# Performance work log

Hardware: AMD Instinct MI355X
Metric: run time of the kernel (lower is better)

Reference implementation:

```python
import jax, jax.numpy as jnp
import numpy as np

N = 524288
L = 16          # num_levels
F = 2           # per_level_dim
T = 1 << 19     # hashmap size per level
BASE, MAXR = 32, 2048
SCALE = np.exp(np.log(MAXR / BASE) / (L - 1))
RES = [int(np.floor(BASE * SCALE ** lv)) + 1 for lv in range(L)]
ACTIVE = 4 * F  # init_active_level * per_level_dim (progressive mask)
D_HID = 64
N_FREQS = 6

_P1 = jnp.uint32(2654435761)
_P2 = jnp.uint32(805459861)
_OFF = jnp.array([[(c >> d) & 1 for d in range(3)] for c in range(8)], dtype=jnp.uint32)  # [8,3]


def setup_inputs() -> dict:
    key = jax.random.key(0)
    ks = jax.random.split(key, 8)
    x = (jax.random.uniform(ks[0], (N, 3)) * 2.0 - 1.0) * 0.999  # inside [-bound, bound]
    v = jax.random.normal(ks[1], (N, 3))
    v = v / jnp.linalg.norm(v, axis=-1, keepdims=True)
    o = jax.random.normal(ks[2], (N, 3))  # unused by forward (kept for signature fidelity)
    table = jax.random.uniform(ks[3], (L, T, F), minval=-1e-4, maxval=1e-4)
    d_in = 3 + 3 * 2 * N_FREQS + L * F  # xyz + fourier + hashgrid = 71
    def lin(k, fi, fo):
        return jax.random.normal(k, (fi, fo)) * np.sqrt(2.0 / fi).astype(np.float32)
    dw1 = lin(ks[4], d_in, D_HID); db1 = jnp.zeros((D_HID,), jnp.float32)
    dw2 = lin(ks[5], D_HID, 1 + D_HID); db2 = jnp.zeros((1 + D_HID,), jnp.float32)
    rw1 = lin(ks[6], D_HID + 9, D_HID); rb1 = jnp.zeros((D_HID,), jnp.float32)
    rw2 = lin(ks[7], D_HID, 3); rb2 = jnp.zeros((3,), jnp.float32)
    return dict(x=x, v=v, o=o, table=table, dw1=dw1, db1=db1, dw2=dw2, db2=db2,
                rw1=rw1, rb1=rb1, rw2=rw2, rb2=rb2)


def hashgrid(x01, table):
    """Multi-res hash encoding with Smoothstep interpolation. x01 in [0,1]^3."""
    feats = []
    for lv in range(L):
        pos = x01 * RES[lv]
        p0 = jnp.floor(pos)
        t = pos - p0
        w = t * t * (3.0 - 2.0 * t)                       # smoothstep weights [N,3]
        corner = p0.astype(jnp.uint32)[:, None, :] + _OFF[None]  # [N,8,3]
        h = (corner[..., 0] ^ (corner[..., 1] * _P1) ^ (corner[..., 2] * _P2)) & jnp.uint32(T - 1)
        cw = jnp.prod(jnp.where(_OFF[None] == 1, w[:, None, :], 1.0 - w[:, None, :]), axis=-1)  # [N,8]
        feats.append(jnp.sum(table[lv][h.astype(jnp.int32)] * cw[..., None], axis=1))  # [N,F]
    return jnp.concatenate(feats, axis=-1)  # [N, L*F]


def fourier(x):
    freqs = 2.0 ** jnp.arange(N_FREQS, dtype=x.dtype)  # log-sampled 2^0..2^5
    ang = x[..., None] * freqs                         # [N,3,6]
    return jnp.concatenate([jnp.sin(ang), jnp.cos(ang)], axis=-1).reshape(x.shape[0], -1)


def sh3(d):
    """Spherical harmonics, degree 3 (levels=3) -> 9 features."""
    xx, yy, zz = d[..., 0], d[..., 1], d[..., 2]
    return jnp.stack([
        0.28209479177387814 * jnp.ones_like(xx),
        -0.4886025119029199 * yy, 0.4886025119029199 * zz, -0.4886025119029199 * xx,
        1.0925484305920792 * xx * yy, -1.0925484305920792 * yy * zz,
        0.9461746957575601 * zz * zz - 0.31539156525252005,
        -1.0925484305920792 * xx * zz,
        0.5462742152960396 * (xx * xx - yy * yy)], axis=-1)


def reference(x, v, o, table, dw1, db1, dw2, db2, rw1, rb1, rw2, rb2):
    x01 = (x + 1.0) * 0.5  # bound = 1.0
    grid = hashgrid(x01, table)
    mask = (jnp.arange(L * F) < ACTIVE).astype(grid.dtype)  # progressive level mask
    x_enc = jnp.concatenate([x, fourier(x), grid * mask], axis=-1)  # [N,71]
    h = jax.nn.relu(x_enc @ dw1 + db1)
    dout = h @ dw2 + db2                 # [N, 1 + d_hidden]
    sigma = jnp.exp(dout[..., :1])       # trunc_exp forward == exp
    feat = jax.nn.relu(dout[..., 1:])
    rgb_in = jnp.concatenate([feat, sh3(v)], axis=-1)  # [N, 73]
    hr = jax.nn.relu(rgb_in @ rw1 + rb1)
    rgb = jax.nn.sigmoid(hr @ rw2 + rb2)
    return sigma, rgb
```

## Files before the change

kernel.cpp:

```cpp
#include <hip/hip_runtime.h>

#define NPTS   524288
#define TBLM   ((1u << 19) - 1u)
#define THR    512
#define CHUNK  128
#define CHUNKS 4
#define GRID   (NPTS / (CHUNK * CHUNKS))

typedef _Float16 half8  __attribute__((ext_vector_type(8)));
typedef _Float16 half4v __attribute__((ext_vector_type(4)));
typedef _Float16 half2v __attribute__((ext_vector_type(2)));
typedef float    f32x4  __attribute__((ext_vector_type(4)));


__global__ __launch_bounds__(256)
void prep(const float* __restrict__ dw1, const float* __restrict__ db1,
          const float* __restrict__ dw2, const float* __restrict__ db2,
          const float* __restrict__ rw1, const float* __restrict__ rb1,
          const float* __restrict__ rw2, const float* __restrict__ rb2,
          void* __restrict__ ws)
{
    const int t = blockIdx.x * 256 + threadIdx.x;
    if (t < 16384) {
        float w = 0.0f;
        if (t < 4096) {
            const int u = t, mkc = u >> 9, m = mkc >> 1, kc = mkc & 1;
            const int lane = (u >> 3) & 63, j = u & 7;
            const int row = 16 * m + (lane & 15);
            const int kp  = kc * 32 + (lane >> 4) * 8 + j;
            if (kp < 39)      w = dw1[kp * 64 + row];
            else if (kp == 39) w = 0.0f;
            else if (kp < 48) w = dw1[(kp - 1) * 64 + row];
        } else if (t < 9216) {
            const int u = t - 4096, mkc = u >> 9, m = mkc >> 1, kc = mkc & 1;
            const int lane = (u >> 3) & 63, j = u & 7;
            const int row = 16 * m + (lane & 15);
            const int k   = kc * 32 + (lane >> 4) * 8 + j;
            if (row < 65) w = dw2[k * 65 + row];
        } else if (t < 15360) {
            const int u = t - 9216, mkc = u >> 9, m = mkc / 3, kc = mkc - 3 * m;
            const int lane = (u >> 3) & 63, j = u & 7;
            const int row = 16 * m + (lane & 15);
            const int kp  = kc * 32 + (lane >> 4) * 8 + j;
            if (kp >= 1 && kp <= 73) w = rw1[(kp - 1) * 64 + row];
        } else {
            const int u = t - 15360, kc = u >> 9;
            const int lane = (u >> 3) & 63, j = u & 7;
            const int row = lane & 15;
            const int k   = kc * 32 + (lane >> 4) * 8 + j;
            if (row < 3) w = rw2[k * 3 + row];
        }
        ((_Float16*)ws)[t] = (_Float16)w;
    } else if (t < 16384 + 224) {
        const int u = t - 16384;
        float b = 0.0f;
        if (u < 64)        b = db1[u];
        else if (u < 144)  { const int r = u - 64;  if (r < 65) b = db2[r]; }
        else if (u < 208)  b = rb1[u - 144];
        else               { const int r = u - 208; if (r < 3)  b = rb2[r]; }
        ((float*)((char*)ws + 32768))[u] = b;
    }
}

__device__ __forceinline__ float sstep(float t) { return t * t * (3.0f - 2.0f * t); }

struct GS {
    float  x0, x1, x2, v0, v1, v2;
    float  ax, ay, az;
    float2 t0, t1, t2, t3, t4, t5, t6, t7;
};

__device__ __forceinline__ void gather_issue(int gi, int role,
    const float* __restrict__ x, const float* __restrict__ v,
    const float* __restrict__ table, GS& s)
{
    s.x0 = x[3 * gi + 0]; s.x1 = x[3 * gi + 1]; s.x2 = x[3 * gi + 2];
    if (role == 1) { s.v0 = v[3 * gi + 0]; s.v1 = v[3 * gi + 1]; s.v2 = v[3 * gi + 2]; }
    const float rf = (role == 0) ? 33.f : (role == 1) ? 43.f : (role == 2) ? 56.f : 74.f;
    const float u0 = (s.x0 + 1.f) * 0.5f, u1 = (s.x1 + 1.f) * 0.5f, u2 = (s.x2 + 1.f) * 0.5f;
    const float px = u0 * rf, py = u1 * rf, pz = u2 * rf;
    const float fx = floorf(px), fy = floorf(py), fz = floorf(pz);
    s.ax = sstep(px - fx); s.ay = sstep(py - fy); s.az = sstep(pz - fz);
    const unsigned cx = (unsigned)fx, cy = (unsigned)fy, cz = (unsigned)fz;
    const float* tb = table + (unsigned)role * (TBLM + 1u) * 2u;
    const unsigned hy0 = cy * 2654435761u, hy1 = (cy + 1u) * 2654435761u;
    const unsigned hz0 = cz * 805459861u,  hz1 = (cz + 1u) * 805459861u;
#define LDC(dst, HX, HY, HZ) { const unsigned hh = ((HX) ^ (HY) ^ (HZ)) & TBLM; \
                               dst = *reinterpret_cast<const float2*>(tb + hh * 2u); }
    LDC(s.t0, cx,      hy0, hz0);
    LDC(s.t1, cx + 1u, hy0, hz0);
    LDC(s.t2, cx,      hy1, hz0);
    LDC(s.t3, cx + 1u, hy1, hz0);
    LDC(s.t4, cx,      hy0, hz1);
    LDC(s.t5, cx + 1u, hy0, hz1);
    LDC(s.t6, cx,      hy1, hz1);
    LDC(s.t7, cx + 1u, hy1, hz1);
#undef LDC
}

__device__ __forceinline__ void encode_finish(const GS& s, int role, _Float16* row)
{
    const float ax = s.ax, ay = s.ay, az = s.az;
    const float bx = 1.f - ax, by = 1.f - ay, bz = 1.f - az;
    const float p00 = bx * by, p10 = ax * by, p01 = bx * ay, p11 = ax * ay;
    const float w0 = p00 * bz, w1 = p10 * bz, w2 = p01 * bz, w3 = p11 * bz;
    const float w4 = p00 * az, w5 = p10 * az, w6 = p01 * az, w7 = p11 * az;
    float g0 = w0 * s.t0.x, g1 = w0 * s.t0.y;
    g0 = fmaf(w1, s.t1.x, g0); g1 = fmaf(w1, s.t1.y, g1);
    g0 = fmaf(w2, s.t2.x, g0); g1 = fmaf(w2, s.t2.y, g1);
    g0 = fmaf(w3, s.t3.x, g0); g1 = fmaf(w3, s.t3.y, g1);
    g0 = fmaf(w4, s.t4.x, g0); g1 = fmaf(w4, s.t4.y, g1);
    g0 = fmaf(w5, s.t5.x, g0); g1 = fmaf(w5, s.t5.y, g1);
    g0 = fmaf(w6, s.t6.x, g0); g1 = fmaf(w6, s.t6.y, g1);
    g0 = fmaf(w7, s.t7.x, g0); g1 = fmaf(w7, s.t7.y, g1);
    half2v gh; gh[0] = (_Float16)g0; gh[1] = (_Float16)g1;
    *(half2v*)(row + 40 + 2 * role) = gh;

    if (role == 0) {
        float e[40];
        e[0] = s.x0; e[1] = s.x1; e[2] = s.x2;
        const float a[3] = {s.x0, s.x1, s.x2};
        #pragma unroll
        for (int d = 0; d < 3; ++d)
            #pragma unroll
            for (int f = 0; f < 6; ++f) {
                const float ang = a[d] * (float)(1 << f);
                e[3 + d * 12 + f]     = __sinf(ang);
                e[3 + d * 12 + 6 + f] = __cosf(ang);
            }
        e[39] = 0.0f;
        #pragma unroll
        for (int chk = 0; chk < 5; ++chk) {
            half8 h;
            #pragma unroll
            for (int i = 0; i < 8; ++i) h[i] = (_Float16)e[chk * 8 + i];
            *(half8*)(row + chk * 8) = h;
        }
    } else if (role == 1) {
        const float v0 = s.v0, v1 = s.v1, v2 = s.v2;
        float sh[9];
        sh[0] = 0.28209479177387814f;
        sh[1] = -0.4886025119029199f * v1;
        sh[2] =  0.4886025119029199f * v2;
        sh[3] = -0.4886025119029199f * v0;
        sh[4] =  1.0925484305920792f * v0 * v1;
        sh[5] = -1.0925484305920792f * v1 * v2;
        sh[6] =  0.9461746957575601f * v2 * v2 - 0.31539156525252005f;
        sh[7] = -1.0925484305920792f * v0 * v2;
        sh[8] =  0.5462742152960396f * (v0 * v0 - v1 * v1);
        half8 s0, s1;
        s0[0] = (_Float16)0.f;
        #pragma unroll
        for (int i = 0; i < 7; ++i) s0[i + 1] = (_Float16)sh[i];
        s1[0] = (_Float16)sh[7]; s1[1] = (_Float16)sh[8];
        #pragma unroll
        for (int i = 2; i < 8; ++i) s1[i] = (_Float16)0.f;
        *(half8*)(row + 64) = s0;
        *(half8*)(row + 72) = s1;
    } else if (role == 2) {
        half8 z;
        #pragma unroll
        for (int i = 0; i < 8; ++i) z[i] = (_Float16)0.f;
        *(half8*)(row + 48) = z;
        *(half8*)(row + 56) = z;
    } else {
        half8 z;
        #pragma unroll
        for (int i = 0; i < 8; ++i) z[i] = (_Float16)0.f;
        *(half8*)(row + 80) = z;
        *(half8*)(row + 88) = z;
    }
}

__global__ __launch_bounds__(THR, 4)
void nerf_fwd(const float* __restrict__ x,
              const float* __restrict__ v,
              const float* __restrict__ table,
              const float* __restrict__ ws,
              float* __restrict__ out)
{
    __shared__ __align__(16) unsigned char smem[78720];
    _Float16* wt    = (_Float16*)smem;
    float*    sbias = (float*)(smem + 32768);
    _Float16* aB    = (_Float16*)(smem + 33664);
    _Float16* bB    = (_Float16*)(smem + 60288);

    const int tid  = threadIdx.x;
    const int lane = tid & 63;
    const int wv   = tid >> 6;
    const int lr   = lane & 15;
    const int lg   = lane >> 4;
    const int role = lane & 3;
    const int ep   = (wv << 4) + (lane >> 2);
    const int gi0  = blockIdx.x * (CHUNK * CHUNKS);

    GS cur, nxt;
    gather_issue(gi0 + ep, role, x, v, table, cur);

    {
        const uint4* src = (const uint4*)ws;
        uint4* dst = (uint4*)smem;
        #pragma unroll
        for (int i = 0; i < 5; ++i) {
            const int idx = tid + i * THR;
            if (idx < 2104) dst[idx] = src[idx];
        }
    }
    __syncthreads();

    const int pt = (wv << 4) + lr;

    #pragma unroll
    for (int c = 0; c < CHUNKS; ++c) {
        const int cbase = gi0 + c * CHUNK;

        encode_finish(cur, role, aB + ep * 104);

        if (c + 1 < CHUNKS)
            gather_issue(gi0 + (c + 1) * CHUNK + ep, role, x, v, table, nxt);

        {
            const half8 B0 = *(const half8*)(aB + pt * 104 + 0 * 32 + lg * 8);
            const half8 B1 = *(const half8*)(aB + pt * 104 + 1 * 32 + lg * 8);
            #pragma unroll
            for (int m = 0; m < 4; ++m) {
                const half8 A0 = *(const half8*)(wt + (m * 2 + 0) * 512 + lane * 8);
                const half8 A1 = *(const half8*)(wt + (m * 2 + 1) * 512 + lane * 8);
                f32x4 cr = *(const f32x4*)(sbias + 0 + m * 16 + 4 * lg);
                cr = __builtin_amdgcn_mfma_f32_16x16x32_f16(A0, B0, cr, 0, 0, 0);
                cr = __builtin_amdgcn_mfma_f32_16x16x32_f16(A1, B1, cr, 0, 0, 0);
                half4v o4;
                #pragma unroll
                for (int r = 0; r < 4; ++r) o4[r] = (_Float16)fmaxf(cr[r], 0.f);
                *(half4v*)(bB + pt * 72 + 16 * m + 4 * lg) = o4;
            }
        }

        {
            const half8 B0 = *(const half8*)(bB + pt * 72 + 0 * 32 + lg * 8);
            const half8 B1 = *(const half8*)(bB + pt * 72 + 1 * 32 + lg * 8);
            #pragma unroll
            for (int m = 0; m < 4; ++m) {
                const half8 A0 = *(const half8*)(wt + 4096 + (m * 2 + 0) * 512 + lane * 8);
                const half8 A1 = *(const half8*)(wt + 4096 + (m * 2 + 1) * 512 + lane * 8);
                f32x4 cr = *(const f32x4*)(sbias + 64 + m * 16 + 4 * lg);
                cr = __builtin_amdgcn_mfma_f32_16x16x32_f16(A0, B0, cr, 0, 0, 0);
                cr = __builtin_amdgcn_mfma_f32_16x16x32_f16(A1, B1, cr, 0, 0, 0);
                half4v o4;
                #pragma unroll
                for (int r = 0; r < 4; ++r) o4[r] = (_Float16)fmaxf(cr[r], 0.f);
                *(half4v*)(aB + pt * 104 + 16 * m + 4 * lg) = o4;
                if (m == 0 && lg == 0)
                    out[cbase + pt] = __expf(cr[0]);
            }
            {
                const half8 A0 = *(const half8*)(wt + 4096 + (4 * 2 + 0) * 512 + lane * 8);
                const half8 A1 = *(const half8*)(wt + 4096 + (4 * 2 + 1) * 512 + lane * 8);
                f32x4 cr = *(const f32x4*)(sbias + 64 + 4 * 16 + 4 * lg);
                cr = __builtin_amdgcn_mfma_f32_16x16x32_f16(A0, B0, cr, 0, 0, 0);
                cr = __builtin_amdgcn_mfma_f32_16x16x32_f16(A1, B1, cr, 0, 0, 0);
                if (lg == 0) aB[pt * 104 + 64] = (_Float16)fmaxf(cr[0], 0.f);
            }
        }

        {
            const half8 B0 = *(const half8*)(aB + pt * 104 + 0 * 32 + lg * 8);
            const half8 B1 = *(const half8*)(aB + pt * 104 + 1 * 32 + lg * 8);
            const half8 B2 = *(const half8*)(aB + pt * 104 + 2 * 32 + lg * 8);
            #pragma unroll
            for (int m = 0; m < 4; ++m) {
                const half8 A0 = *(const half8*)(wt + 9216 + (m * 3 + 0) * 512 + lane * 8);
                const half8 A1 = *(const half8*)(wt + 9216 + (m * 3 + 1) * 512 + lane * 8);
                const half8 A2 = *(const half8*)(wt + 9216 + (m * 3 + 2) * 512 + lane * 8);
                f32x4 cr = *(const f32x4*)(sbias + 144 + m * 16 + 4 * lg);
                cr = __builtin_amdgcn_mfma_f32_16x16x32_f16(A0, B0, cr, 0, 0, 0);
                cr = __builtin_amdgcn_mfma_f32_16x16x32_f16(A1, B1, cr, 0, 0, 0);
                cr = __builtin_amdgcn_mfma_f32_16x16x32_f16(A2, B2, cr, 0, 0, 0);
                half4v o4;
                #pragma unroll
                for (int r = 0; r < 4; ++r) o4[r] = (_Float16)fmaxf(cr[r], 0.f);
                *(half4v*)(bB + pt * 72 + 16 * m + 4 * lg) = o4;
            }
        }

        {
            const half8 A0 = *(const half8*)(wt + 15360 + 0 * 512 + lane * 8);
            const half8 A1 = *(const half8*)(wt + 15360 + 1 * 512 + lane * 8);
            const half8 B0 = *(const half8*)(bB + pt * 72 + 0 * 32 + lg * 8);
            const half8 B1 = *(const half8*)(bB + pt * 72 + 1 * 32 + lg * 8);
            f32x4 cr = *(const f32x4*)(sbias + 208 + 4 * lg);
            cr = __builtin_amdgcn_mfma_f32_16x16x32_f16(A0, B0, cr, 0, 0, 0);
            cr = __builtin_amdgcn_mfma_f32_16x16x32_f16(A1, B1, cr, 0, 0, 0);
            if (lg == 0) {
                const int gpt = cbase + pt;
                #pragma unroll
                for (int r = 0; r < 3; ++r)
                    out[NPTS + 3 * gpt + r] = 1.0f / (1.0f + __expf(-cr[r]));
            }
        }

        if (c + 1 < CHUNKS) cur = nxt;
    }
}

extern "C" void kernel_launch(void* const* d_in, const int* in_sizes, int n_in,
                              void* d_out, int out_size, void* d_ws, size_t ws_size,
                              hipStream_t stream) {
    const float* x     = (const float*)d_in[0];
    const float* v     = (const float*)d_in[1];
    const float* table = (const float*)d_in[3];
    const float* dw1   = (const float*)d_in[4];
    const float* db1   = (const float*)d_in[5];
    const float* dw2   = (const float*)d_in[6];
    const float* db2   = (const float*)d_in[7];
    const float* rw1   = (const float*)d_in[8];
    const float* rb1   = (const float*)d_in[9];
    const float* rw2   = (const float*)d_in[10];
    const float* rb2   = (const float*)d_in[11];
    float* out = (float*)d_out;

    hipLaunchKernelGGL(prep, dim3(65), dim3(256), 0, stream,
                       dw1, db1, dw2, db2, rw1, rb1, rw2, rb2, d_ws);
    hipLaunchKernelGGL(nerf_fwd, dim3(GRID), dim3(THR), 0, stream,
                       x, v, table, (const float*)d_ws, out);
}
```

Before: 187.8 us.

## Hold MLP weights in registers and shrink blocks to 256 threads

Loads all fp16 MLP weight fragments into per-lane registers once per block instead of reading them from LDS for every MFMA. LDS now holds only the biases and the activation buffers. Blocks shrink to 256 threads with 8 chunks of 64 points, and launch bounds drop to 2 blocks per CU. The zero-padding of activation rows is hoisted out of the per-chunk encode into a single pre-loop step. The aim is to cut LDS traffic and LDS footprint, at the cost of about 100 extra VGPRs per lane, which lowers occupancy and the latency hiding available for the hash-table gathers.

```diff
diff --git a/kernel.cpp b/kernel.cpp
--- a/kernel.cpp
+++ b/kernel.cpp
@@ -2,9 +2,9 @@
 
 #define NPTS   524288
 #define TBLM   ((1u << 19) - 1u)
-#define THR    512
-#define CHUNK  128
-#define CHUNKS 4
+#define THR    256
+#define CHUNK  64
+#define CHUNKS 8
 #define GRID   (NPTS / (CHUNK * CHUNKS))
 
 typedef _Float16 half8  __attribute__((ext_vector_type(8)));
@@ -157,33 +157,20 @@
         for (int i = 2; i < 8; ++i) s1[i] = (_Float16)0.f;
         *(half8*)(row + 64) = s0;
         *(half8*)(row + 72) = s1;
-    } else if (role == 2) {
-        half8 z;
-        #pragma unroll
-        for (int i = 0; i < 8; ++i) z[i] = (_Float16)0.f;
-        *(half8*)(row + 48) = z;
-        *(half8*)(row + 56) = z;
-    } else {
-        half8 z;
-        #pragma unroll
-        for (int i = 0; i < 8; ++i) z[i] = (_Float16)0.f;
-        *(half8*)(row + 80) = z;
-        *(half8*)(row + 88) = z;
     }
 }
 
-__global__ __launch_bounds__(THR, 4)
+__global__ __launch_bounds__(THR, 2)
 void nerf_fwd(const float* __restrict__ x,
               const float* __restrict__ v,
               const float* __restrict__ table,
               const float* __restrict__ ws,
               float* __restrict__ out)
 {
-    __shared__ __align__(16) unsigned char smem[78720];
-    _Float16* wt    = (_Float16*)smem;
-    float*    sbias = (float*)(smem + 32768);
-    _Float16* aB    = (_Float16*)(smem + 33664);
-    _Float16* bB    = (_Float16*)(smem + 60288);
+    __shared__ __align__(16) unsigned char smem[23424];
+    float*    sbias = (float*)smem;
+    _Float16* aB    = (_Float16*)(smem + 896);
+    _Float16* bB    = (_Float16*)(smem + 14208);
 
     const int tid  = threadIdx.x;
     const int lane = tid & 63;
@@ -197,20 +184,42 @@
     GS cur, nxt;
     gather_issue(gi0 + ep, role, x, v, table, cur);
 
+    const _Float16* wsH = (const _Float16*)ws;
+    half8 W1[4][2], W2[5][2], W3[4][3], W4[2];
+    #pragma unroll
+    for (int m = 0; m < 4; ++m)
+        #pragma unroll
+        for (int kc = 0; kc < 2; ++kc)
+            W1[m][kc] = *(const half8*)(wsH + (m * 2 + kc) * 512 + lane * 8);
+    #pragma unroll
+    for (int m = 0; m < 5; ++m)
+        #pragma unroll
+        for (int kc = 0; kc < 2; ++kc)
+            W2[m][kc] = *(const half8*)(wsH + 4096 + (m * 2 + kc) * 512 + lane * 8);
+    #pragma unroll
+    for (int m = 0; m < 4; ++m)
+        #pragma unroll
+        for (int kc = 0; kc < 3; ++kc)
+            W3[m][kc] = *(const half8*)(wsH + 9216 + (m * 3 + kc) * 512 + lane * 8);
+    #pragma unroll
+    for (int kc = 0; kc < 2; ++kc)
+        W4[kc] = *(const half8*)(wsH + 15360 + kc * 512 + lane * 8);
+
+    if (tid < 56) ((uint4*)sbias)[tid] = ((const uint4*)((const char*)ws + 32768))[tid];
+    __syncthreads();
+
     {
-        const uint4* src = (const uint4*)ws;
-        uint4* dst = (uint4*)smem;
-        #pragma unroll
-        for (int i = 0; i < 5; ++i) {
-            const int idx = tid + i * THR;
-            if (idx < 2104) dst[idx] = src[idx];
-        }
+        _Float16* rowp = aB + ep * 104;
+        half8 z;
+        #pragma unroll
+        for (int i = 0; i < 8; ++i) z[i] = (_Float16)0.f;
+        *(half8*)(rowp + 48 + 8 * role) = z;
+        if (role < 2) *(half8*)(rowp + 80 + 8 * role) = z;
     }
-    __syncthreads();
 
     const int pt = (wv << 4) + lr;
 
-    #pragma unroll
+    #pragma unroll 2
     for (int c = 0; c < CHUNKS; ++c) {
         const int cbase = gi0 + c * CHUNK;
 
@@ -224,11 +233,9 @@
             const half8 B1 = *(const half8*)(aB + pt * 104 + 1 * 32 + lg * 8);
             #pragma unroll
             for (int m = 0; m < 4; ++m) {
-                const half8 A0 = *(const half8*)(wt + (m * 2 + 0) * 512 + lane * 8);
-                const half8 A1 = *(const half8*)(wt + (m * 2 + 1) * 512 + lane * 8);
                 f32x4 cr = *(const f32x4*)(sbias + 0 + m * 16 + 4 * lg);
-                cr = __builtin_amdgcn_mfma_f32_16x16x32_f16(A0, B0, cr, 0, 0, 0);
-                cr = __builtin_amdgcn_mfma_f32_16x16x32_f16(A1, B1, cr, 0, 0, 0);
+                cr = __builtin_amdgcn_mfma_f32_16x16x32_f16(W1[m][0], B0, cr, 0, 0, 0);
+                cr = __builtin_amdgcn_mfma_f32_16x16x32_f16(W1[m][1], B1, cr, 0, 0, 0);
                 half4v o4;
                 #pragma unroll
                 for (int r = 0; r < 4; ++r) o4[r] = (_Float16)fmaxf(cr[r], 0.f);
@@ -241,11 +248,9 @@
             const half8 B1 = *(const half8*)(bB + pt * 72 + 1 * 32 + lg * 8);
             #pragma unroll
             for (int m = 0; m < 4; ++m) {
-                const half8 A0 = *(const half8*)(wt + 4096 + (m * 2 + 0) * 512 + lane * 8);
-                const half8 A1 = *(const half8*)(wt + 4096 + (m * 2 + 1) * 512 + lane * 8);
                 f32x4 cr = *(const f32x4*)(sbias + 64 + m * 16 + 4 * lg);
-                cr = __builtin_amdgcn_mfma_f32_16x16x32_f16(A0, B0, cr, 0, 0, 0);
-                cr = __builtin_amdgcn_mfma_f32_16x16x32_f16(A1, B1, cr, 0, 0, 0);
+                cr = __builtin_amdgcn_mfma_f32_16x16x32_f16(W2[m][0], B0, cr, 0, 0, 0);
+                cr = __builtin_amdgcn_mfma_f32_16x16x32_f16(W2[m][1], B1, cr, 0, 0, 0);
                 half4v o4;
                 #pragma unroll
                 for (int r = 0; r < 4; ++r) o4[r] = (_Float16)fmaxf(cr[r], 0.f);
@@ -254,11 +259,9 @@
                     out[cbase + pt] = __expf(cr[0]);
             }
             {
-                const half8 A0 = *(const half8*)(wt + 4096 + (4 * 2 + 0) * 512 + lane * 8);
-                const half8 A1 = *(const half8*)(wt + 4096 + (4 * 2 + 1) * 512 + lane * 8);
                 f32x4 cr = *(const f32x4*)(sbias + 64 + 4 * 16 + 4 * lg);
-                cr = __builtin_amdgcn_mfma_f32_16x16x32_f16(A0, B0, cr, 0, 0, 0);
-                cr = __builtin_amdgcn_mfma_f32_16x16x32_f16(A1, B1, cr, 0, 0, 0);
+                cr = __builtin_amdgcn_mfma_f32_16x16x32_f16(W2[4][0], B0, cr, 0, 0, 0);
+                cr = __builtin_amdgcn_mfma_f32_16x16x32_f16(W2[4][1], B1, cr, 0, 0, 0);
                 if (lg == 0) aB[pt * 104 + 64] = (_Float16)fmaxf(cr[0], 0.f);
             }
         }
@@ -269,13 +272,10 @@
             const half8 B2 = *(const half8*)(aB + pt * 104 + 2 * 32 + lg * 8);
             #pragma unroll
             for (int m = 0; m < 4; ++m) {
-                const half8 A0 = *(const half8*)(wt + 9216 + (m * 3 + 0) * 512 + lane * 8);
-                const half8 A1 = *(const half8*)(wt + 9216 + (m * 3 + 1) * 512 + lane * 8);
-                const half8 A2 = *(const half8*)(wt + 9216 + (m * 3 + 2) * 512 + lane * 8);
                 f32x4 cr = *(const f32x4*)(sbias + 144 + m * 16 + 4 * lg);
-                cr = __builtin_amdgcn_mfma_f32_16x16x32_f16(A0, B0, cr, 0, 0, 0);
-                cr = __builtin_amdgcn_mfma_f32_16x16x32_f16(A1, B1, cr, 0, 0, 0);
-                cr = __builtin_amdgcn_mfma_f32_16x16x32_f16(A2, B2, cr, 0, 0, 0);
+                cr = __builtin_amdgcn_mfma_f32_16x16x32_f16(W3[m][0], B0, cr, 0, 0, 0);
+                cr = __builtin_amdgcn_mfma_f32_16x16x32_f16(W3[m][1], B1, cr, 0, 0, 0);
+                cr = __builtin_amdgcn_mfma_f32_16x16x32_f16(W3[m][2], B2, cr, 0, 0, 0);
                 half4v o4;
                 #pragma unroll
                 for (int r = 0; r < 4; ++r) o4[r] = (_Float16)fmaxf(cr[r], 0.f);
@@ -284,13 +284,11 @@
         }
 
         {
-            const half8 A0 = *(const half8*)(wt + 15360 + 0 * 512 + lane * 8);
-            const half8 A1 = *(const half8*)(wt + 15360 + 1 * 512 + lane * 8);
             const half8 B0 = *(const half8*)(bB + pt * 72 + 0 * 32 + lg * 8);
             const half8 B1 = *(const half8*)(bB + pt * 72 + 1 * 32 + lg * 8);
             f32x4 cr = *(const f32x4*)(sbias + 208 + 4 * lg);
-            cr = __builtin_amdgcn_mfma_f32_16x16x32_f16(A0, B0, cr, 0, 0, 0);
-            cr = __builtin_amdgcn_mfma_f32_16x16x32_f16(A1, B1, cr, 0, 0, 0);
+            cr = __builtin_amdgcn_mfma_f32_16x16x32_f16(W4[0], B0, cr, 0, 0, 0);
+            cr = __builtin_amdgcn_mfma_f32_16x16x32_f16(W4[1], B1, cr, 0, 0, 0);
             if (lg == 0) {
                 const int gpt = cbase + pt;
                 #pragma unroll
```

After: 194.9 us. 1.04x slower.
